# Kernel optimization log

Hardware: AMD Instinct MI355X
Metric: run time of the kernel (lower is better)

## Reference

```python
import jax, jax.numpy as jnp
import numpy as np

B, S, D, P, W = 16, 100, 8192, 100, 3  # batch, seq, feat dim, proj width, window size


def setup_inputs() -> dict:
    key = jax.random.key(0)
    ks = jax.random.split(key, 6)
    return {
        "x": jax.random.normal(ks[0], (B, S, D), dtype=jnp.float32),
        "wq": jax.random.normal(ks[1], (D, P), dtype=jnp.float32) * (1.0 / np.sqrt(D)),
        "wk": jax.random.normal(ks[2], (D, P), dtype=jnp.float32) * (1.0 / np.sqrt(D)),
        "wv": jax.random.normal(ks[3], (D, P), dtype=jnp.float32) * (1.0 / np.sqrt(D)),
        "forwardpad": jax.random.normal(ks[4], (B, 1, D), dtype=jnp.float32),
        "backwardpad": jax.random.normal(ks[5], (B, 1, D), dtype=jnp.float32),
    }


def reference(x, wq, wk, wv, forwardpad, backwardpad):
    # pad: (B, S+2, D)
    padded = jnp.concatenate([forwardpad, x, backwardpad], axis=1)
    # gather all 100 overlapping size-3 windows at once: (B, S, W, D)
    idx = jnp.arange(S)[:, None] + jnp.arange(W)[None, :]  # (S, W)
    windows = padded[:, idx, :]
    # shared projections across all windows (original recomputed per window)
    q = jnp.einsum("bswd,dp->bswp", windows, wq)
    k = jnp.einsum("bswd,dp->bswp", windows, wk)
    v = jnp.einsum("bswd,dp->bswp", windows, wv)
    # per-window 3x3 attention
    scores = jnp.einsum("bswp,bsup->bswu", q, k)  # (B, S, W, W)
    attn = jax.nn.softmax(scores, axis=-1)
    out = jnp.einsum("bswu,bsup->bswp", attn, v)  # (B, S, W, P)
    # original concatenates windows along seq then takes [:, 1::3, :] -> center token of each window
    return out[:, :, 1, :]  # (B, S, P)
```

## Files before the change

kernel.cpp:

```cpp
#include <hip/hip_runtime.h>
#include <hip/hip_bf16.h>
#include <hip/hip_fp16.h>

constexpr int Dk   = 8192;
constexpr int Bb   = 16;
constexpr int Ss   = 100;
constexpr int Pp   = 100;
constexpr int MROW = 1632;
constexpr int NT   = 20;
constexpr int NCC  = 320;
constexpr int NQ   = 304;
constexpr int KG   = 1024;
constexpr int KC   = 32;
constexpr int CH   = 5;
constexpr int MBL2 = 26;

constexpr size_t B_SEG   = (size_t)NT * KG * 128;
constexpr size_t PSTRIDE = (size_t)1664 * NCC;

typedef short s8v __attribute__((ext_vector_type(8)));
typedef float f4v __attribute__((ext_vector_type(4)));

__device__ inline unsigned short f2bf_rne(float f) {
    unsigned u = __float_as_uint(f);
    u += 0x7fffu + ((u >> 16) & 1u);
    return (unsigned short)(u >> 16);
}

__global__ __launch_bounds__(256) void pack_b(
    const float* __restrict__ wq, const float* __restrict__ wk,
    const float* __restrict__ wv,
    short* __restrict__ b_hi, short* __restrict__ b_lo) {
    const int id = blockIdx.x * 256 + threadIdx.x;
    const int n  = id % NCC;
    const int kg = id / NCC;
    if (kg >= KG) return;

    const float* w = nullptr; int p = 0;
    if (n < 100)      { w = wq; p = n; }
    else if (n < 200) { w = wk; p = n - 100; }
    else if (n < 300) { w = wv; p = n - 200; }

    s8v hi, lo;
    #pragma unroll
    for (int j = 0; j < 8; ++j) {
        const float v = w ? w[(size_t)(kg * 8 + j) * Pp + p] : 0.0f;
        const unsigned u = __float_as_uint(v);
        hi[j] = (short)(unsigned short)(u >> 16);
        const float hf = __uint_as_float(u & 0xffff0000u);
        lo[j] = (short)f2bf_rne(v - hf);
    }
    const size_t doff = ((size_t)(n >> 4) * KG + kg) * 128 + (size_t)(n & 15) * 8;
    *(s8v*)(b_hi + doff) = hi;
    *(s8v*)(b_lo + doff) = lo;
}

__global__ __launch_bounds__(256, 2) void qkv_gemm(
    const float* __restrict__ x, const float* __restrict__ fpad,
    const float* __restrict__ bpad,
    const short* __restrict__ b_hi, const short* __restrict__ b_lo,
    unsigned short* __restrict__ part) {
    __shared__ __align__(16) short ahi[16384];
    __shared__ __align__(16) short alo[16384];

    const int id   = blockIdx.x;
    const int xcd  = id & 7;
    const int slot = id >> 3;
    const int sub  = slot & 3;
    const int kc   = xcd * 4 + sub;
    const int mb   = slot >> 2;

    const int tid  = threadIdx.x;
    const int w    = tid >> 6;
    const int l    = tid & 63;
    const int m    = l & 15;
    const int quad = l >> 4;

    const int sr  = tid >> 2;
    const int skq = tid & 3;
    const float* sp;
    {
        const int r = mb * 64 + sr;
        if (r >= MROW) sp = fpad;
        else {
            const int b = r / 102, rr = r - b * 102;
            if (rr == 0)        sp = fpad + (size_t)b * Dk;
            else if (rr == 101) sp = bpad + (size_t)b * Dk;
            else                sp = x + ((size_t)b * Ss + (rr - 1)) * Dk;
        }
        sp += kc * 256 + skq * 8;
    }

    #pragma unroll
    for (int it = 0; it < 8; ++it) {
        const float4 v0 = *(const float4*)(sp + it * 32);
        const float4 v1 = *(const float4*)(sp + it * 32 + 4);
        const float vv[8] = {v0.x, v0.y, v0.z, v0.w, v1.x, v1.y, v1.z, v1.w};
        s8v h8, l8;
        #pragma unroll
        for (int jj = 0; jj < 8; ++jj) {
            const unsigned u = __float_as_uint(vv[jj]);
            h8[jj] = (short)(unsigned short)(u >> 16);
            l8[jj] = (short)f2bf_rne(vv[jj] - __uint_as_float(u & 0xffff0000u));
        }
        const int off = (((sr >> 4) * 32 + it * 4 + skq) * 16 + (sr & 15)) * 8;
        *(s8v*)&ahi[off] = h8;
        *(s8v*)&alo[off] = l8;
    }
    __syncthreads();

    s8v bh[2][5], bl[2][5];
    {
        const int kg0 = kc * 32 + quad;
        #pragma unroll
        for (int j = 0; j < 5; ++j) {
            const size_t bo = ((size_t)(w * 5 + j) * KG + kg0) * 128 + (size_t)m * 8;
            bh[0][j] = *(const s8v*)(b_hi + bo);
            bl[0][j] = *(const s8v*)(b_lo + bo);
        }
    }

    f4v acc[4][5];
    #pragma unroll
    for (int i = 0; i < 4; ++i)
        #pragma unroll
        for (int j = 0; j < 5; ++j) {
            f4v z = {0.f, 0.f, 0.f, 0.f};
            acc[i][j] = z;
        }

    #pragma unroll
    for (int s = 0; s < 8; ++s) {
        const int cur = s & 1, nxt = cur ^ 1;

        if (s < 7) {
            const int kgn = kc * 32 + (s + 1) * 4 + quad;
            #pragma unroll
            for (int j = 0; j < 5; ++j) {
                const size_t bo = ((size_t)(w * 5 + j) * KG + kgn) * 128 + (size_t)m * 8;
                bh[nxt][j] = *(const s8v*)(b_hi + bo);
                bl[nxt][j] = *(const s8v*)(b_lo + bo);
            }
        }

        s8v ah[4], al[4];
        #pragma unroll
        for (int i = 0; i < 4; ++i) {
            const int ao = ((i * 32 + s * 4 + quad) * 16 + m) * 8;
            ah[i] = *(const s8v*)&ahi[ao];
            al[i] = *(const s8v*)&alo[ao];
        }

        #pragma unroll
        for (int j = 0; j < 5; ++j) {
            const s8v bhv = bh[cur][j], blv = bl[cur][j];
            #pragma unroll
            for (int i = 0; i < 4; ++i)
                acc[i][j] = __builtin_amdgcn_mfma_f32_16x16x32_bf16(ah[i], bhv, acc[i][j], 0, 0, 0);
            #pragma unroll
            for (int i = 0; i < 4; ++i)
                acc[i][j] = __builtin_amdgcn_mfma_f32_16x16x32_bf16(al[i], bhv, acc[i][j], 0, 0, 0);
            #pragma unroll
            for (int i = 0; i < 4; ++i)
                acc[i][j] = __builtin_amdgcn_mfma_f32_16x16x32_bf16(ah[i], blv, acc[i][j], 0, 0, 0);
        }
    }

    unsigned short* __restrict__ pout = part + (size_t)kc * PSTRIDE;
    #pragma unroll
    for (int i = 0; i < 4; ++i) {
        #pragma unroll
        for (int j = 0; j < 5; ++j) {
            const int col  = (w * 5 + j) * 16 + m;
            const int row0 = mb * 64 + i * 16 + quad * 4;
            #pragma unroll
            for (int r = 0; r < 4; ++r)
                pout[(size_t)(row0 + r) * NCC + col] =
                    __half_as_ushort(__float2half(acc[i][j][r]));
        }
    }
}

__global__ __launch_bounds__(256) void reduce_k(
    const unsigned short* __restrict__ part, float* __restrict__ qkv) {
    const int t = blockIdx.x * 256 + threadIdx.x;
    const int row = t / 40;
    const int col0 = (t - row * 40) * 8;
    const size_t base = (size_t)row * NCC + col0;

    float sum[8] = {0.f, 0.f, 0.f, 0.f, 0.f, 0.f, 0.f, 0.f};
    #pragma unroll
    for (int k = 0; k < KC; ++k) {
        const s8v u = *(const s8v*)(part + (size_t)k * PSTRIDE + base);
        #pragma unroll
        for (int ii = 0; ii < 8; ++ii)
            sum[ii] += __half2float(__ushort_as_half((unsigned short)u[ii]));
    }
    if (col0 < NQ) {
        f4v a = {sum[0], sum[1], sum[2], sum[3]};
        f4v b = {sum[4], sum[5], sum[6], sum[7]};
        *(f4v*)(qkv + (size_t)row * NQ + col0)     = a;
        *(f4v*)(qkv + (size_t)row * NQ + col0 + 4) = b;
    }
}

__global__ __launch_bounds__(256) void attn3(
    const float* __restrict__ qkv, float* __restrict__ out) {
    const int blk = blockIdx.x;
    const int b  = blk / (Ss / CH);
    const int c  = blk % (Ss / CH);
    const int s0 = c * CH;
    const int tid = threadIdx.x;

    __shared__ float red[CH + 2][304];
    __shared__ float sc[CH][3];

    for (int idx = tid; idx < (CH + 2) * 300; idx += 256) {
        const int row = idx / 300, col = idx % 300;
        red[row][col] = qkv[(size_t)(b * 102 + s0 + row) * NQ + col];
    }
    __syncthreads();

    if (tid < CH * 3 * 16) {
        const int d = tid >> 4, g = tid & 15;
        const int ss = d / 3, u = d % 3;
        float ps = 0.0f;
        #pragma unroll
        for (int t = 0; t < 7; ++t) {
            const int p = g + t * 16;
            if (p < Pp) ps += red[ss + 1][p] * red[ss + u][100 + p];
        }
        #pragma unroll
        for (int off = 8; off > 0; off >>= 1) ps += __shfl_down(ps, off, 16);
        if (g == 0) sc[ss][u] = ps;
    }
    __syncthreads();

    for (int idx = tid; idx < CH * Pp; idx += 256) {
        const int ss = idx / Pp, p = idx % Pp;
        const float a0 = sc[ss][0], a1 = sc[ss][1], a2 = sc[ss][2];
        const float mx = fmaxf(a0, fmaxf(a1, a2));
        const float e0 = __expf(a0 - mx), e1 = __expf(a1 - mx), e2 = __expf(a2 - mx);
        const float inv = 1.0f / (e0 + e1 + e2);
        out[(size_t)(b * Ss + s0 + ss) * Pp + p] =
            inv * (e0 * red[ss][200 + p] + e1 * red[ss + 1][200 + p] +
                   e2 * red[ss + 2][200 + p]);
    }
}

extern "C" void kernel_launch(void* const* d_in, const int* in_sizes, int n_in,
                              void* d_out, int out_size, void* d_ws, size_t ws_size,
                              hipStream_t stream) {
    const float* x    = (const float*)d_in[0];
    const float* wq   = (const float*)d_in[1];
    const float* wk   = (const float*)d_in[2];
    const float* wv   = (const float*)d_in[3];
    const float* fpad = (const float*)d_in[4];
    const float* bpad = (const float*)d_in[5];
    float* out = (float*)d_out;

    short* b_hi = (short*)d_ws;
    short* b_lo = b_hi + B_SEG;
    unsigned short* part = (unsigned short*)(b_lo + B_SEG);
    float* qkv = (float*)(part + (size_t)KC * PSTRIDE);

    pack_b<<<(NCC * KG) / 256, 256, 0, stream>>>(wq, wk, wv, b_hi, b_lo);
    qkv_gemm<<<MBL2 * KC, 256, 0, stream>>>(x, fpad, bpad, b_hi, b_lo, part);
    reduce_k<<<260, 256, 0, stream>>>(part, qkv);
    attn3<<<Bb * (Ss / CH), 256, 0, stream>>>(qkv, out);
}
```

Measured before the change: 143.9 us.

## Enlarge GEMM tile to 128 rows with 512 threads and halve split-K

The QKV GEMM block grows from 64 to 128 rows using 8 waves in a 2x4 arrangement, and the split-K factor drops from 32 to 16. Each block now covers 512 K elements in two halves that are staged in sequence through LDS. This doubles reuse of the B fragments across M and halves the partial-sum traffic written by the GEMM and read back by reduce_k. In exchange the grid shrinks from 832 to 208 blocks and each block uses more LDS, which lowers occupancy and parallelism. Staging the second half sits between barriers and is not overlapped with compute.

```diff
diff --git a/kernel.cpp b/kernel.cpp
--- a/kernel.cpp
+++ b/kernel.cpp
@@ -11,9 +11,9 @@
 constexpr int NCC  = 320;
 constexpr int NQ   = 304;
 constexpr int KG   = 1024;
-constexpr int KC   = 32;
+constexpr int KC   = 16;
 constexpr int CH   = 5;
-constexpr int MBL2 = 26;
+constexpr int MBL3 = 13;
 
 constexpr size_t B_SEG   = (size_t)NT * KG * 128;
 constexpr size_t PSTRIDE = (size_t)1664 * NCC;
@@ -55,23 +55,25 @@
     *(s8v*)(b_lo + doff) = lo;
 }
 
-__global__ __launch_bounds__(256, 2) void qkv_gemm(
+__global__ __launch_bounds__(512) void qkv_gemm(
     const float* __restrict__ x, const float* __restrict__ fpad,
     const float* __restrict__ bpad,
     const short* __restrict__ b_hi, const short* __restrict__ b_lo,
     unsigned short* __restrict__ part) {
-    __shared__ __align__(16) short ahi[16384];
-    __shared__ __align__(16) short alo[16384];
+    __shared__ __align__(16) short ahi[32768];
+    __shared__ __align__(16) short alo[32768];
 
     const int id   = blockIdx.x;
     const int xcd  = id & 7;
     const int slot = id >> 3;
-    const int sub  = slot & 3;
-    const int kc   = xcd * 4 + sub;
-    const int mb   = slot >> 2;
+    const int sub  = slot & 1;
+    const int kc   = xcd * 2 + sub;
+    const int mb   = slot >> 1;
 
     const int tid  = threadIdx.x;
     const int w    = tid >> 6;
+    const int wm   = w >> 2;
+    const int wn   = w & 3;
     const int l    = tid & 63;
     const int m    = l & 15;
     const int quad = l >> 4;
@@ -80,7 +82,7 @@
     const int skq = tid & 3;
     const float* sp;
     {
-        const int r = mb * 64 + sr;
+        const int r = mb * 128 + sr;
         if (r >= MROW) sp = fpad;
         else {
             const int b = r / 102, rr = r - b * 102;
@@ -88,33 +90,38 @@
             else if (rr == 101) sp = bpad + (size_t)b * Dk;
             else                sp = x + ((size_t)b * Ss + (rr - 1)) * Dk;
         }
-        sp += kc * 256 + skq * 8;
-    }
-
-    #pragma unroll
-    for (int it = 0; it < 8; ++it) {
-        const float4 v0 = *(const float4*)(sp + it * 32);
-        const float4 v1 = *(const float4*)(sp + it * 32 + 4);
-        const float vv[8] = {v0.x, v0.y, v0.z, v0.w, v1.x, v1.y, v1.z, v1.w};
-        s8v h8, l8;
-        #pragma unroll
-        for (int jj = 0; jj < 8; ++jj) {
-            const unsigned u = __float_as_uint(vv[jj]);
-            h8[jj] = (short)(unsigned short)(u >> 16);
-            l8[jj] = (short)f2bf_rne(vv[jj] - __uint_as_float(u & 0xffff0000u));
-        }
-        const int off = (((sr >> 4) * 32 + it * 4 + skq) * 16 + (sr & 15)) * 8;
-        *(s8v*)&ahi[off] = h8;
-        *(s8v*)&alo[off] = l8;
-    }
-    __syncthreads();
+        sp += kc * 512 + skq * 8;
+    }
+    const int wbase = ((sr >> 4) * 32 + skq) * 16 + (sr & 15);
+
+    auto stage_half = [&](int h) {
+        #pragma unroll
+        for (int it = 0; it < 8; ++it) {
+            const float4 v0 = *(const float4*)(sp + h * 256 + it * 32);
+            const float4 v1 = *(const float4*)(sp + h * 256 + it * 32 + 4);
+            const float vv[8] = {v0.x, v0.y, v0.z, v0.w, v1.x, v1.y, v1.z, v1.w};
+            s8v h8, l8;
+            #pragma unroll
+            for (int jj = 0; jj < 8; ++jj) {
+                const unsigned u = __float_as_uint(vv[jj]);
+                h8[jj] = (short)(unsigned short)(u >> 16);
+                l8[jj] = (short)f2bf_rne(vv[jj] - __uint_as_float(u & 0xffff0000u));
+            }
+            const int off = (wbase + it * 64) * 8;
+            *(s8v*)&ahi[off] = h8;
+            *(s8v*)&alo[off] = l8;
+        }
+    };
+
+    stage_half(0);
+    asm volatile("s_waitcnt lgkmcnt(0)\n\ts_barrier" ::: "memory");
 
     s8v bh[2][5], bl[2][5];
     {
-        const int kg0 = kc * 32 + quad;
+        const int kg0 = kc * 64 + quad;
         #pragma unroll
         for (int j = 0; j < 5; ++j) {
-            const size_t bo = ((size_t)(w * 5 + j) * KG + kg0) * 128 + (size_t)m * 8;
+            const size_t bo = ((size_t)(wn * 5 + j) * KG + kg0) * 128 + (size_t)m * 8;
             bh[0][j] = *(const s8v*)(b_hi + bo);
             bl[0][j] = *(const s8v*)(b_lo + bo);
         }
@@ -130,49 +137,59 @@
         }
 
     #pragma unroll
-    for (int s = 0; s < 8; ++s) {
-        const int cur = s & 1, nxt = cur ^ 1;
-
-        if (s < 7) {
-            const int kgn = kc * 32 + (s + 1) * 4 + quad;
+    for (int h = 0; h < 2; ++h) {
+        #pragma unroll
+        for (int s = 0; s < 8; ++s) {
+            const int t   = h * 8 + s;
+            const int cur = t & 1, nxt = cur ^ 1;
+
+            if (t < 15) {
+                const int tn = t + 1;
+                const int kgn = kc * 64 + (tn >> 3) * 32 + (tn & 7) * 4 + quad;
+                #pragma unroll
+                for (int j = 0; j < 5; ++j) {
+                    const size_t bo = ((size_t)(wn * 5 + j) * KG + kgn) * 128 + (size_t)m * 8;
+                    bh[nxt][j] = *(const s8v*)(b_hi + bo);
+                    bl[nxt][j] = *(const s8v*)(b_lo + bo);
+                }
+            }
+
+            s8v ah[4], al[4];
+            #pragma unroll
+            for (int i = 0; i < 4; ++i) {
+                const int ao = (((wm * 4 + i) * 32 + s * 4 + quad) * 16 + m) * 8;
+                ah[i] = *(const s8v*)&ahi[ao];
+                al[i] = *(const s8v*)&alo[ao];
+            }
+
             #pragma unroll
             for (int j = 0; j < 5; ++j) {
-                const size_t bo = ((size_t)(w * 5 + j) * KG + kgn) * 128 + (size_t)m * 8;
-                bh[nxt][j] = *(const s8v*)(b_hi + bo);
-                bl[nxt][j] = *(const s8v*)(b_lo + bo);
-            }
-        }
-
-        s8v ah[4], al[4];
-        #pragma unroll
-        for (int i = 0; i < 4; ++i) {
-            const int ao = ((i * 32 + s * 4 + quad) * 16 + m) * 8;
-            ah[i] = *(const s8v*)&ahi[ao];
-            al[i] = *(const s8v*)&alo[ao];
-        }
-
+                const s8v bhv = bh[cur][j], blv = bl[cur][j];
+                #pragma unroll
+                for (int i = 0; i < 4; ++i)
+                    acc[i][j] = __builtin_amdgcn_mfma_f32_16x16x32_bf16(ah[i], bhv, acc[i][j], 0, 0, 0);
+                #pragma unroll
+                for (int i = 0; i < 4; ++i)
+                    acc[i][j] = __builtin_amdgcn_mfma_f32_16x16x32_bf16(al[i], bhv, acc[i][j], 0, 0, 0);
+                #pragma unroll
+                for (int i = 0; i < 4; ++i)
+                    acc[i][j] = __builtin_amdgcn_mfma_f32_16x16x32_bf16(ah[i], blv, acc[i][j], 0, 0, 0);
+            }
+        }
+        if (h == 0) {
+            asm volatile("s_waitcnt lgkmcnt(0)\n\ts_barrier" ::: "memory");
+            stage_half(1);
+            asm volatile("s_waitcnt lgkmcnt(0)\n\ts_barrier" ::: "memory");
+        }
+    }
+
+    unsigned short* __restrict__ pout = part + (size_t)kc * PSTRIDE;
+    #pragma unroll
+    for (int i = 0; i < 4; ++i) {
         #pragma unroll
         for (int j = 0; j < 5; ++j) {
-            const s8v bhv = bh[cur][j], blv = bl[cur][j];
-            #pragma unroll
-            for (int i = 0; i < 4; ++i)
-                acc[i][j] = __builtin_amdgcn_mfma_f32_16x16x32_bf16(ah[i], bhv, acc[i][j], 0, 0, 0);
-            #pragma unroll
-            for (int i = 0; i < 4; ++i)
-                acc[i][j] = __builtin_amdgcn_mfma_f32_16x16x32_bf16(al[i], bhv, acc[i][j], 0, 0, 0);
-            #pragma unroll
-            for (int i = 0; i < 4; ++i)
-                acc[i][j] = __builtin_amdgcn_mfma_f32_16x16x32_bf16(ah[i], blv, acc[i][j], 0, 0, 0);
-        }
-    }
-
-    unsigned short* __restrict__ pout = part + (size_t)kc * PSTRIDE;
-    #pragma unroll
-    for (int i = 0; i < 4; ++i) {
-        #pragma unroll
-        for (int j = 0; j < 5; ++j) {
-            const int col  = (w * 5 + j) * 16 + m;
-            const int row0 = mb * 64 + i * 16 + quad * 4;
+            const int col  = (wn * 5 + j) * 16 + m;
+            const int row0 = mb * 128 + (wm * 4 + i) * 16 + quad * 4;
             #pragma unroll
             for (int r = 0; r < 4; ++r)
                 pout[(size_t)(row0 + r) * NCC + col] =
@@ -265,7 +282,7 @@
     float* qkv = (float*)(part + (size_t)KC * PSTRIDE);
 
     pack_b<<<(NCC * KG) / 256, 256, 0, stream>>>(wq, wk, wv, b_hi, b_lo);
-    qkv_gemm<<<MBL2 * KC, 256, 0, stream>>>(x, fpad, bpad, b_hi, b_lo, part);
+    qkv_gemm<<<MBL3 * KC, 512, 0, stream>>>(x, fpad, bpad, b_hi, b_lo, part);
     reduce_k<<<260, 256, 0, stream>>>(part, qkv);
     attn3<<<Bb * (Ss / CH), 256, 0, stream>>>(qkv, out);
 }
```

Measured after the change: 137.2 us. -4.6%, faster.

## Load A operand directly from global into registers, dropping LDS staging

Applied to the files above, without the earlier changes.

The GEMM kernel no longer stages the x rows through shared memory. Each lane now loads its own A fragments from global memory every k-step and splits them into hi/lo bf16 in registers. This removes the LDS writes, the barrier and the LDS reads. The residual lo part is now truncated instead of round-to-nearest, which slightly changes precision. The occupancy hint of 2 blocks is dropped, and the global loads are less coalesced and no longer overlapped ahead of use.

```diff
diff --git a/kernel.cpp b/kernel.cpp
--- a/kernel.cpp
+++ b/kernel.cpp
@@ -55,14 +55,11 @@
     *(s8v*)(b_lo + doff) = lo;
 }
 
-__global__ __launch_bounds__(256, 2) void qkv_gemm(
+__global__ __launch_bounds__(256) void qkv_gemm(
     const float* __restrict__ x, const float* __restrict__ fpad,
     const float* __restrict__ bpad,
     const short* __restrict__ b_hi, const short* __restrict__ b_lo,
     unsigned short* __restrict__ part) {
-    __shared__ __align__(16) short ahi[16384];
-    __shared__ __align__(16) short alo[16384];
-
     const int id   = blockIdx.x;
     const int xcd  = id & 7;
     const int slot = id >> 3;
@@ -76,38 +73,20 @@
     const int m    = l & 15;
     const int quad = l >> 4;
 
-    const int sr  = tid >> 2;
-    const int skq = tid & 3;
-    const float* sp;
-    {
-        const int r = mb * 64 + sr;
-        if (r >= MROW) sp = fpad;
+    const float* ap[4];
+    #pragma unroll
+    for (int i = 0; i < 4; ++i) {
+        const int r = mb * 64 + i * 16 + m;
+        const float* p;
+        if (r >= MROW) p = fpad;
         else {
             const int b = r / 102, rr = r - b * 102;
-            if (rr == 0)        sp = fpad + (size_t)b * Dk;
-            else if (rr == 101) sp = bpad + (size_t)b * Dk;
-            else                sp = x + ((size_t)b * Ss + (rr - 1)) * Dk;
-        }
-        sp += kc * 256 + skq * 8;
-    }
-
-    #pragma unroll
-    for (int it = 0; it < 8; ++it) {
-        const float4 v0 = *(const float4*)(sp + it * 32);
-        const float4 v1 = *(const float4*)(sp + it * 32 + 4);
-        const float vv[8] = {v0.x, v0.y, v0.z, v0.w, v1.x, v1.y, v1.z, v1.w};
-        s8v h8, l8;
-        #pragma unroll
-        for (int jj = 0; jj < 8; ++jj) {
-            const unsigned u = __float_as_uint(vv[jj]);
-            h8[jj] = (short)(unsigned short)(u >> 16);
-            l8[jj] = (short)f2bf_rne(vv[jj] - __uint_as_float(u & 0xffff0000u));
-        }
-        const int off = (((sr >> 4) * 32 + it * 4 + skq) * 16 + (sr & 15)) * 8;
-        *(s8v*)&ahi[off] = h8;
-        *(s8v*)&alo[off] = l8;
-    }
-    __syncthreads();
+            if (rr == 0)        p = fpad + (size_t)b * Dk;
+            else if (rr == 101) p = bpad + (size_t)b * Dk;
+            else                p = x + ((size_t)b * Ss + (rr - 1)) * Dk;
+        }
+        ap[i] = p + kc * 256 + quad * 8;
+    }
 
     s8v bh[2][5], bl[2][5];
     {
@@ -132,6 +111,13 @@
     #pragma unroll
     for (int s = 0; s < 8; ++s) {
         const int cur = s & 1, nxt = cur ^ 1;
+
+        f4v a0[4], a1[4];
+        #pragma unroll
+        for (int i = 0; i < 4; ++i) {
+            a0[i] = *(const f4v*)(ap[i] + s * 32);
+            a1[i] = *(const f4v*)(ap[i] + s * 32 + 4);
+        }
 
         if (s < 7) {
             const int kgn = kc * 32 + (s + 1) * 4 + quad;
@@ -146,9 +132,17 @@
         s8v ah[4], al[4];
         #pragma unroll
         for (int i = 0; i < 4; ++i) {
-            const int ao = ((i * 32 + s * 4 + quad) * 16 + m) * 8;
-            ah[i] = *(const s8v*)&ahi[ao];
-            al[i] = *(const s8v*)&alo[ao];
+            #pragma unroll
+            for (int jj = 0; jj < 4; ++jj) {
+                const unsigned u0 = __float_as_uint(a0[i][jj]);
+                ah[i][jj] = (short)(unsigned short)(u0 >> 16);
+                const float t0 = a0[i][jj] - __uint_as_float(u0 & 0xffff0000u);
+                al[i][jj] = (short)(unsigned short)(__float_as_uint(t0) >> 16);
+                const unsigned u1 = __float_as_uint(a1[i][jj]);
+                ah[i][4 + jj] = (short)(unsigned short)(u1 >> 16);
+                const float t1 = a1[i][jj] - __uint_as_float(u1 & 0xffff0000u);
+                al[i][4 + jj] = (short)(unsigned short)(__float_as_uint(t1) >> 16);
+            }
         }
 
         #pragma unroll
```

Result: slower. 168.8 us (+17.3%).
